# Kernel tuning notes

Hardware: AMD Instinct MI355X
Metric: run time of the kernel (lower is better)

Reference implementation:

```python
import jax, jax.numpy as jnp
import numpy as np

B, S, D, H = 2, 2048, 1024, 16
DH = D // H


def setup_inputs() -> dict:
    key = jax.random.key(0)
    ks = jax.random.split(key, 13)
    s = 1.0 / np.sqrt(D)
    inp = {
        "q": jax.random.normal(ks[0], (B, S, D), jnp.float32),
        "k": jax.random.normal(ks[1], (B, S, D), jnp.float32),
        "v": jax.random.normal(ks[2], (B, S, D), jnp.float32),
        # causal mask [B,1,Q,K]: True = attend
        "attn_mask": jnp.broadcast_to(jnp.tril(jnp.ones((S, S), bool))[None, None], (B, 1, S, S)),
        "rel_bias": 0.1 * jax.random.normal(ks[3], (H, S, S), jnp.float32),
        "Wq": s * jax.random.normal(ks[4], (D, D), jnp.float32),
        "bq": jnp.zeros((D,), jnp.float32),
        "Wk": s * jax.random.normal(ks[5], (D, D), jnp.float32),
        "bk": jnp.zeros((D,), jnp.float32),
        "Wv": s * jax.random.normal(ks[6], (D, D), jnp.float32),
        "bv": jnp.zeros((D,), jnp.float32),
        "Wo": s * jax.random.normal(ks[7], (D, D), jnp.float32),
        "bo": jnp.zeros((D,), jnp.float32),
    }
    return inp


def reference(q, k, v, attn_mask, rel_bias, Wq, bq, Wk, bk, Wv, bv, Wo, bo):
    Bq, Q, Dm = q.shape
    K = k.shape[1]
    # projections -> [B, H, S, DH]
    qh = (q @ Wq + bq).reshape(Bq, Q, H, DH).transpose(0, 2, 1, 3)
    kh = (k @ Wk + bk).reshape(Bq, K, H, DH).transpose(0, 2, 1, 3)
    vh = (v @ Wv + bv).reshape(Bq, K, H, DH).transpose(0, 2, 1, 3)
    scores = jnp.einsum("bhqd,bhkd->bhqk", qh, kh) / np.sqrt(DH).astype(np.float32)
    scores = scores + rel_bias  # [H,Q,K] broadcasts over batch
    scores = jnp.where(attn_mask, scores, -jnp.inf)
    attn = jax.nn.softmax(scores, axis=-1)
    out = jnp.einsum("bhqk,bhkd->bhqd", attn, vh)
    out = out.transpose(0, 2, 1, 3).reshape(Bq, Q, Dm)
    return out @ Wo + bo
```

## Files before the change

### kernel.cpp

```cpp
#include <hip/hip_runtime.h>

typedef unsigned short u16;
typedef __attribute__((ext_vector_type(8))) short bf16x8;
typedef __attribute__((ext_vector_type(4))) float f32x4;
typedef __attribute__((ext_vector_type(4))) unsigned short us4;

#define B_ 2
#define S_ 2048
#define D_ 1024
#define H_ 16
#define DH_ 64
#define M_ 4096

__device__ __forceinline__ u16 f2bf(float f) {
  unsigned int u = __builtin_bit_cast(unsigned int, f);
  u += 0x7FFFu + ((u >> 16) & 1u);
  return (u16)(u >> 16);
}

__device__ __forceinline__ unsigned int cvtpk(float lo, float hi) {
  unsigned int r;
  asm("v_cvt_pk_bf16_f32 %0, %1, %2" : "=v"(r) : "v"(lo), "v"(hi));
  return r;
}

__device__ __forceinline__ float fexp2(float x) {
  float r;
  asm("v_exp_f32 %0, %1" : "=v"(r) : "v"(x));
  return r;
}

__device__ __forceinline__ void gload_lds16(const void* g, void* l) {
  __builtin_amdgcn_global_load_lds(
      (__attribute__((address_space(1))) void*)(g),
      (__attribute__((address_space(3))) void*)(l),
      16, 0, 0);
}

__global__ __launch_bounds__(256) void wprep_kernel(const float* __restrict__ W0,
                                                    const float* __restrict__ W1,
                                                    const float* __restrict__ W2,
                                                    const float* __restrict__ W3,
                                                    u16* __restrict__ Wt,
                                                    const float* __restrict__ qin,
                                                    const float* __restrict__ kin,
                                                    const float* __restrict__ vin,
                                                    u16* __restrict__ Xq,
                                                    u16* __restrict__ Xk,
                                                    u16* __restrict__ Xv) {
  int z = blockIdx.z;
  if (z < 4) {
    __shared__ float tile[32][33];
    const float* W = (z == 0) ? W0 : (z == 1) ? W1 : (z == 2) ? W2 : W3;
    u16* out = Wt + (size_t)z * D_ * D_;
    int tx = threadIdx.x, ty = threadIdx.y;
    int x = blockIdx.x * 32 + tx;
    for (int j = 0; j < 32; j += 8)
      tile[ty + j][tx] = W[(size_t)(blockIdx.y * 32 + ty + j) * D_ + x];
    __syncthreads();
    int x2 = blockIdx.y * 32 + tx;
    for (int j = 0; j < 32; j += 8)
      out[(size_t)(blockIdx.x * 32 + ty + j) * D_ + x2] = f2bf(tile[tx][ty + j]);
  } else {
    int zz = z - 4;
    const float* src = (zz == 0) ? qin : (zz == 1) ? kin : vin;
    u16* dst = (zz == 0) ? Xq : (zz == 1) ? Xk : Xv;
    int bid = blockIdx.y * 32 + blockIdx.x;
    int t = threadIdx.y * 32 + threadIdx.x;
    const float4* s4 = (const float4*)src;
    for (int i = 0; i < 4; ++i) {
      int idx = bid * 1024 + i * 256 + t;
      float4 v4 = s4[idx];
      us4 o;
      o[0] = f2bf(v4.x); o[1] = f2bf(v4.y); o[2] = f2bf(v4.z); o[3] = f2bf(v4.w);
      ((us4*)dst)[idx] = o;
    }
  }
}

__global__ __launch_bounds__(256) void gemm_qkv(const u16* __restrict__ Xq,
                                                const u16* __restrict__ Xk,
                                                const u16* __restrict__ Xv,
                                                const u16* __restrict__ Wt,
                                                const float* __restrict__ bq,
                                                const float* __restrict__ bk,
                                                const float* __restrict__ bv,
                                                u16* __restrict__ Qh,
                                                u16* __restrict__ Kh,
                                                u16* __restrict__ Vt) {
  __shared__ u16 As[128 * 32];
  __shared__ u16 Bs[128 * 32];
  int fid = blockIdx.x;
  int xcd = fid & 7, ii = fid >> 3;
  int grp = ii >> 3, yy = ii & 7;
  int gg = xcd * 12 + grp;
  int z = gg >> 5;
  int xx = gg & 31;
  const u16* A = (z == 0) ? Xq : (z == 1) ? Xk : Xv;
  const u16* Bt = Wt + (size_t)z * D_ * D_;
  const float* bias = (z == 0) ? bq : (z == 1) ? bk : bv;
  u16* O = (z == 0) ? Qh : (z == 1) ? Kh : Vt;

  int tid = threadIdx.x;
  int lane = tid & 63, wave = tid >> 6;
  int m0 = xx * 128, n0 = yy * 128;
  int wr = wave >> 1, wc = wave & 1;
  int fr = lane & 15, fk = (lane >> 4) * 8;

  f32x4 acc[4][4];
  const f32x4 vzero = {0.f, 0.f, 0.f, 0.f};
  for (int i = 0; i < 4; ++i)
    for (int j = 0; j < 4; ++j) acc[i][j] = vzero;

  for (int k0 = 0; k0 < D_; k0 += 32) {
    if (k0) __syncthreads();
    for (int i = 0; i < 2; ++i) {
      int wofs = ((i * 4 + wave) << 10);
      int ofs = wofs + lane * 16;
      int row = ofs >> 6;
      int cole = (ofs & 63) >> 1;
      gload_lds16(A + (size_t)(m0 + row) * D_ + k0 + cole, (char*)As + wofs);
      gload_lds16(Bt + (size_t)(n0 + row) * D_ + k0 + cole, (char*)Bs + wofs);
    }
    __syncthreads();
    bf16x8 af[4], bfr[4];
    for (int mi = 0; mi < 4; ++mi)
      af[mi] = *(const bf16x8*)(As + (wr * 64 + mi * 16 + fr) * 32 + fk);
    for (int ni = 0; ni < 4; ++ni)
      bfr[ni] = *(const bf16x8*)(Bs + (wc * 64 + ni * 16 + fr) * 32 + fk);
    for (int mi = 0; mi < 4; ++mi)
      for (int ni = 0; ni < 4; ++ni)
        acc[mi][ni] =
            __builtin_amdgcn_mfma_f32_16x16x32_bf16(af[mi], bfr[ni], acc[mi][ni], 0, 0, 0);
  }

  if (z == 2) {
    for (int mi = 0; mi < 4; ++mi) {
      int rowb = m0 + wr * 64 + mi * 16 + (lane >> 4) * 4;
      int bb2 = rowb >> 11, s0 = rowb & (S_ - 1);
      for (int ni = 0; ni < 4; ++ni) {
        int col = n0 + wc * 64 + ni * 16 + fr;
        int hh = col >> 6, dh = col & 63;
        float bv = bias[col];
        us4 pk;
        for (int r = 0; r < 4; ++r) pk[r] = f2bf(acc[mi][ni][r] + bv);
        *(us4*)(O + ((size_t)(bb2 * H_ + hh) * DH_ + dh) * S_ + s0) = pk;
      }
    }
  } else {
    float scale = (z == 0) ? 0.125f : 1.0f;
    for (int mi = 0; mi < 4; ++mi) {
      int rowb = m0 + wr * 64 + mi * 16 + (lane >> 4) * 4;
      for (int ni = 0; ni < 4; ++ni) {
        int col = n0 + wc * 64 + ni * 16 + fr;
        int hh = col >> 6, dh = col & 63;
        float bv = bias[col];
        for (int r = 0; r < 4; ++r) {
          int row = rowb + r;
          int bb2 = row >> 11, s = row & (S_ - 1);
          O[((size_t)(bb2 * H_ + hh) * S_ + s) * DH_ + dh] =
              f2bf((acc[mi][ni][r] + bv) * scale);
        }
      }
    }
  }
}

__global__ __launch_bounds__(256) void gemm_out(const u16* __restrict__ A,
                                                const u16* __restrict__ Bt,
                                                const float* __restrict__ bias,
                                                float* __restrict__ O) {
  __shared__ u16 As[64 * 32];
  __shared__ u16 Bs[128 * 32];
  int fid = blockIdx.x;
  int xcd = fid & 7, ii = fid >> 3;
  int grp = ii >> 3, yy = ii & 7;
  int gg = xcd * 8 + grp;
  int tid = threadIdx.x;
  int lane = tid & 63, wave = tid >> 6;
  int m0 = gg * 64, n0 = yy * 128;
  int fr = lane & 15, fk = (lane >> 4) * 8;

  f32x4 acc[4][2];
  const f32x4 vzero = {0.f, 0.f, 0.f, 0.f};
  for (int i = 0; i < 4; ++i)
    for (int j = 0; j < 2; ++j) acc[i][j] = vzero;

  for (int k0 = 0; k0 < D_; k0 += 32) {
    if (k0) __syncthreads();
    {
      int wofs = wave << 10;
      int ofs = wofs + lane * 16;
      int row = ofs >> 6;
      int cole = (ofs & 63) >> 1;
      gload_lds16(A + (size_t)(m0 + row) * D_ + k0 + cole, (char*)As + wofs);
    }
    for (int i = 0; i < 2; ++i) {
      int wofs = ((i * 4 + wave) << 10);
      int ofs = wofs + lane * 16;
      int row = ofs >> 6;
      int cole = (ofs & 63) >> 1;
      gload_lds16(Bt + (size_t)(n0 + row) * D_ + k0 + cole, (char*)Bs + wofs);
    }
    __syncthreads();
    bf16x8 af[4], bfr[2];
    for (int mi = 0; mi < 4; ++mi)
      af[mi] = *(const bf16x8*)(As + (mi * 16 + fr) * 32 + fk);
    for (int ni = 0; ni < 2; ++ni)
      bfr[ni] = *(const bf16x8*)(Bs + (wave * 32 + ni * 16 + fr) * 32 + fk);
    for (int mi = 0; mi < 4; ++mi)
      for (int ni = 0; ni < 2; ++ni)
        acc[mi][ni] =
            __builtin_amdgcn_mfma_f32_16x16x32_bf16(af[mi], bfr[ni], acc[mi][ni], 0, 0, 0);
  }

  for (int mi = 0; mi < 4; ++mi) {
    int rowb = m0 + mi * 16 + (lane >> 4) * 4;
    for (int ni = 0; ni < 2; ++ni) {
      int col = n0 + wave * 32 + ni * 16 + fr;
      float bv = bias[col];
      for (int r = 0; r < 4; ++r)
        O[(size_t)(rowb + r) * D_ + col] = acc[mi][ni][r] + bv;
    }
  }
}

__global__ __launch_bounds__(256, 4) void attn_kernel(const u16* __restrict__ Qh,
                                                      const u16* __restrict__ Kh,
                                                      const u16* __restrict__ Vt,
                                                      const float* __restrict__ relb,
                                                      u16* __restrict__ attnout) {
  __shared__ u16 KVs[2][2][4096];

  int fid = blockIdx.x;
  int rr = fid >> 8, c = fid & 255;
  int j = c >> 3, e = c & 7;
  int s = (rr & 1) ? j : 31 - j;
  int h = (rr & 1) ? e + 8 : e;
  int b = rr >> 1;

  int w = threadIdx.x >> 6, lane = threadIdx.x & 63;
  int fr = lane & 15, g = lane >> 4;
  int q0w = s * 64 + w * 16;
  int qme = q0w + fr;
  int bh = b * H_ + h;
  int sx = (fr & 7) << 4;

  int kind = w >> 1;
  int i0 = (w & 1) * 4;
  int srow_lo = lane >> 3;
  int scb = (lane & 7) * 16;

  const u16* Qb = Qh + ((size_t)bh * S_ + q0w) * DH_;
  bf16x8 qf0 = *(const bf16x8*)(Qb + fr * DH_ + 8 * g);
  bf16x8 qf1 = *(const bf16x8*)(Qb + fr * DH_ + 32 + 8 * g);

  const float* Bq = relb + (size_t)h * S_ * S_ + (size_t)qme * S_ + 4 * g;
  const float LOG2E = 1.44269504f;

  int T = s + 1;

  auto STAGE = [&](int buf, int kb) {
    for (int i = 0; i < 4; ++i) {
      int ii = i0 + i;
      int row = ii * 8 + srow_lo;
      int cbs = scb ^ ((row & 7) << 4);
      const u16* src;
      if (kind == 0)
        src = Kh + ((size_t)bh * S_ + kb + row) * DH_ + (cbs >> 1);
      else
        src = Vt + ((size_t)bh * DH_ + row) * S_ + kb + (cbs >> 1);
      gload_lds16(src, &KVs[kind][buf][ii * 512]);
    }
  };

  f32x4 acc[4];
  const f32x4 vzero = {0.f, 0.f, 0.f, 0.f};
  for (int f4 = 0; f4 < 4; ++f4) acc[f4] = vzero;
  float m = -1.0e4f, l = 0.f;

  STAGE(0, 0);
  f32x4 bi[4], bn[4];
  for (int cc = 0; cc < 4; ++cc) bi[cc] = *(const f32x4*)(Bq + 16 * cc);
  __syncthreads();

  for (int t = 0; t < T; ++t) {
    int kb = t * 64;
    int buf = t & 1;
    bool diag = (t == T - 1);
    if (!diag) {
      STAGE(buf ^ 1, kb + 64);
      for (int cc = 0; cc < 4; ++cc) bn[cc] = *(const f32x4*)(Bq + kb + 64 + 16 * cc);
    }

    const u16* Kt = &KVs[0][buf][0];
    const u16* Vl = &KVs[1][buf][0];

    f32x4 sc[4];
    __builtin_amdgcn_s_setprio(1);
    for (int cc = 0; cc < 4; ++cc) {
      bf16x8 k0 = *(const bf16x8*)(Kt + (16 * cc + fr) * 64 + (((16 * g) ^ sx) >> 1));
      bf16x8 k1 = *(const bf16x8*)(Kt + (16 * cc + fr) * 64 + (((64 + 16 * g) ^ sx) >> 1));
      f32x4 z = __builtin_amdgcn_mfma_f32_16x16x32_bf16(k0, qf0, bi[cc], 0, 0, 0);
      z = __builtin_amdgcn_mfma_f32_16x16x32_bf16(k1, qf1, z, 0, 0, 0);
      sc[cc] = z;
    }
    __builtin_amdgcn_s_setprio(0);
    if (diag) {
      for (int cc = 0; cc < 4; ++cc)
        for (int r = 0; r < 4; ++r) {
          int key = kb + 16 * cc + 4 * g + r;
          sc[cc][r] = (key <= qme) ? sc[cc][r] : -1e30f;
        }
    }
    float pm = sc[0][0];
    for (int cc = 0; cc < 4; ++cc)
      for (int r = 0; r < 4; ++r) pm = fmaxf(pm, sc[cc][r]);
    pm = fmaxf(pm, __shfl_xor(pm, 16));
    pm = fmaxf(pm, __shfl_xor(pm, 32));
    if (!__all(pm - m <= 8.0f)) {
      float mn = fmaxf(m, pm);
      float corr = __expf(m - mn);
      m = mn;
      l *= corr;
      float c0 = __shfl(corr, 4 * g + 0);
      float c1 = __shfl(corr, 4 * g + 1);
      float c2 = __shfl(corr, 4 * g + 2);
      float c3 = __shfl(corr, 4 * g + 3);
      for (int f4 = 0; f4 < 4; ++f4) {
        acc[f4][0] *= c0; acc[f4][1] *= c1; acc[f4][2] *= c2; acc[f4][3] *= c3;
      }
    }
    float nms = m * -LOG2E;
    float rs = 0.f;
    for (int cc = 0; cc < 4; ++cc)
      for (int r = 0; r < 4; ++r) {
        sc[cc][r] = fexp2(fmaf(sc[cc][r], LOG2E, nms));
        rs += sc[cc][r];
      }
    l += rs;
    union { unsigned int w4[4]; bf16x8 v; } pp[2];
    for (int jj = 0; jj < 2; ++jj) {
      pp[jj].w4[0] = cvtpk(sc[2 * jj][0], sc[2 * jj][1]);
      pp[jj].w4[1] = cvtpk(sc[2 * jj][2], sc[2 * jj][3]);
      pp[jj].w4[2] = cvtpk(sc[2 * jj + 1][0], sc[2 * jj + 1][1]);
      pp[jj].w4[3] = cvtpk(sc[2 * jj + 1][2], sc[2 * jj + 1][3]);
    }
    __builtin_amdgcn_s_setprio(1);
    for (int f4 = 0; f4 < 4; ++f4) {
      for (int jj = 0; jj < 2; ++jj) {
        union { us4 hh[2]; bf16x8 v; } vf;
        vf.hh[0] = *(const us4*)(Vl + (f4 * 16 + fr) * 64 + (((jj * 64 + 8 * g) ^ sx) >> 1));
        vf.hh[1] = *(const us4*)(Vl + (f4 * 16 + fr) * 64 + (((jj * 64 + 32 + 8 * g) ^ sx) >> 1));
        acc[f4] = __builtin_amdgcn_mfma_f32_16x16x32_bf16(pp[jj].v, vf.v, acc[f4], 0, 0, 0);
      }
    }
    __builtin_amdgcn_s_setprio(0);
    for (int cc = 0; cc < 4; ++cc) bi[cc] = bn[cc];
    __syncthreads();
  }

  l += __shfl_xor(l, 16);
  l += __shfl_xor(l, 32);
  float il = 1.f / l;
  for (int r = 0; r < 4; ++r) {
    float ilr = __shfl(il, 4 * g + r);
    int qq = q0w + 4 * g + r;
    u16* ob = attnout + ((size_t)b * S_ + qq) * D_ + h * 64;
    for (int f4 = 0; f4 < 4; ++f4) ob[f4 * 16 + fr] = f2bf(acc[f4][r] * ilr);
  }
}

extern "C" void kernel_launch(void* const* d_in, const int* in_sizes, int n_in,
                              void* d_out, int out_size, void* d_ws, size_t ws_size,
                              hipStream_t stream) {
  const float* q = (const float*)d_in[0];
  const float* k = (const float*)d_in[1];
  const float* v = (const float*)d_in[2];
  const float* rb = (const float*)d_in[4];
  const float* Wq = (const float*)d_in[5];
  const float* bq = (const float*)d_in[6];
  const float* Wk = (const float*)d_in[7];
  const float* bk = (const float*)d_in[8];
  const float* Wv = (const float*)d_in[9];
  const float* bv = (const float*)d_in[10];
  const float* Wo = (const float*)d_in[11];
  const float* bo = (const float*)d_in[12];
  float* out = (float*)d_out;

  char* ws = (char*)d_ws;
  const size_t SZ = (size_t)M_ * D_ * 2;
  u16* Xq = (u16*)(ws);
  u16* Xk = (u16*)(ws + SZ);
  u16* Xv = (u16*)(ws + 2 * SZ);
  u16* Qh = (u16*)(ws + 3 * SZ);
  u16* Kh = (u16*)(ws + 4 * SZ);
  u16* Vt = (u16*)(ws + 5 * SZ);
  u16* Wt = (u16*)(ws + 6 * SZ);
  u16* Xb = Xq;

  wprep_kernel<<<dim3(32, 32, 7), dim3(32, 8), 0, stream>>>(Wq, Wk, Wv, Wo, Wt,
                                                            q, k, v, Xq, Xk, Xv);

  gemm_qkv<<<dim3(768), 256, 0, stream>>>(Xq, Xk, Xv, Wt, bq, bk, bv, Qh, Kh, Vt);

  attn_kernel<<<dim3(1024), 256, 0, stream>>>(Qh, Kh, Vt, rb, Xb);

  gemm_out<<<dim3(512), 256, 0, stream>>>(Xb, Wt + 3 * (size_t)D_ * D_, bo, out);
}
```

Baseline: 142.5 us.

## Load K/V fragments directly from global into registers, dropping LDS staging

The attention kernel no longer stages K and V tiles into shared memory with async global-to-LDS copies and block barriers. Each wave now loads its own K and V MFMA fragments straight from global memory into registers, prefetching the next K tile while the current one is used. Launch bounds drop from 4 to 3 blocks per CU to make room for the extra registers. The cost is that all four waves read the same K/V data redundantly from global or L2, with narrower, less coalesced V loads and lower occupancy, in exchange for removing the barriers and LDS traffic.

Measured after the change: 363.9 us. 155% more time.

```diff
diff --git a/kernel.cpp b/kernel.cpp
--- a/kernel.cpp
+++ b/kernel.cpp
@@ -225,13 +225,11 @@
   }
 }
 
-__global__ __launch_bounds__(256, 4) void attn_kernel(const u16* __restrict__ Qh,
+__global__ __launch_bounds__(256, 3) void attn_kernel(const u16* __restrict__ Qh,
                                                       const u16* __restrict__ Kh,
                                                       const u16* __restrict__ Vt,
                                                       const float* __restrict__ relb,
                                                       u16* __restrict__ attnout) {
-  __shared__ u16 KVs[2][2][4096];
-
   int fid = blockIdx.x;
   int rr = fid >> 8, c = fid & 255;
   int j = c >> 3, e = c & 7;
@@ -244,68 +242,62 @@
   int q0w = s * 64 + w * 16;
   int qme = q0w + fr;
   int bh = b * H_ + h;
-  int sx = (fr & 7) << 4;
-
-  int kind = w >> 1;
-  int i0 = (w & 1) * 4;
-  int srow_lo = lane >> 3;
-  int scb = (lane & 7) * 16;
 
   const u16* Qb = Qh + ((size_t)bh * S_ + q0w) * DH_;
   bf16x8 qf0 = *(const bf16x8*)(Qb + fr * DH_ + 8 * g);
   bf16x8 qf1 = *(const bf16x8*)(Qb + fr * DH_ + 32 + 8 * g);
 
+  const u16* Kp = Kh + ((size_t)bh * S_ + fr) * DH_ + 8 * g;
+  const u16* Vp = Vt + ((size_t)bh * DH_ + fr) * S_ + 4 * g;
   const float* Bq = relb + (size_t)h * S_ * S_ + (size_t)qme * S_ + 4 * g;
   const float LOG2E = 1.44269504f;
 
   int T = s + 1;
-
-  auto STAGE = [&](int buf, int kb) {
-    for (int i = 0; i < 4; ++i) {
-      int ii = i0 + i;
-      int row = ii * 8 + srow_lo;
-      int cbs = scb ^ ((row & 7) << 4);
-      const u16* src;
-      if (kind == 0)
-        src = Kh + ((size_t)bh * S_ + kb + row) * DH_ + (cbs >> 1);
-      else
-        src = Vt + ((size_t)bh * DH_ + row) * S_ + kb + (cbs >> 1);
-      gload_lds16(src, &KVs[kind][buf][ii * 512]);
-    }
-  };
 
   f32x4 acc[4];
   const f32x4 vzero = {0.f, 0.f, 0.f, 0.f};
   for (int f4 = 0; f4 < 4; ++f4) acc[f4] = vzero;
   float m = -1.0e4f, l = 0.f;
 
-  STAGE(0, 0);
+  bf16x8 kf0[4], kf1[4];
+  for (int cc = 0; cc < 4; ++cc) {
+    kf0[cc] = *(const bf16x8*)(Kp + (size_t)(16 * cc) * DH_);
+    kf1[cc] = *(const bf16x8*)(Kp + (size_t)(16 * cc) * DH_ + 32);
+  }
   f32x4 bi[4], bn[4];
   for (int cc = 0; cc < 4; ++cc) bi[cc] = *(const f32x4*)(Bq + 16 * cc);
-  __syncthreads();
 
   for (int t = 0; t < T; ++t) {
     int kb = t * 64;
-    int buf = t & 1;
     bool diag = (t == T - 1);
-    if (!diag) {
-      STAGE(buf ^ 1, kb + 64);
-      for (int cc = 0; cc < 4; ++cc) bn[cc] = *(const f32x4*)(Bq + kb + 64 + 16 * cc);
-    }
-
-    const u16* Kt = &KVs[0][buf][0];
-    const u16* Vl = &KVs[1][buf][0];
+
+    us4 vf[4][4];
+    for (int f4 = 0; f4 < 4; ++f4) {
+      const u16* vrow = Vp + (size_t)(f4 * 16) * S_ + kb;
+      vf[f4][0] = *(const us4*)(vrow);
+      vf[f4][1] = *(const us4*)(vrow + 16);
+      vf[f4][2] = *(const us4*)(vrow + 32);
+      vf[f4][3] = *(const us4*)(vrow + 48);
+    }
 
     f32x4 sc[4];
     __builtin_amdgcn_s_setprio(1);
     for (int cc = 0; cc < 4; ++cc) {
-      bf16x8 k0 = *(const bf16x8*)(Kt + (16 * cc + fr) * 64 + (((16 * g) ^ sx) >> 1));
-      bf16x8 k1 = *(const bf16x8*)(Kt + (16 * cc + fr) * 64 + (((64 + 16 * g) ^ sx) >> 1));
-      f32x4 z = __builtin_amdgcn_mfma_f32_16x16x32_bf16(k0, qf0, bi[cc], 0, 0, 0);
-      z = __builtin_amdgcn_mfma_f32_16x16x32_bf16(k1, qf1, z, 0, 0, 0);
+      f32x4 z = __builtin_amdgcn_mfma_f32_16x16x32_bf16(kf0[cc], qf0, bi[cc], 0, 0, 0);
+      z = __builtin_amdgcn_mfma_f32_16x16x32_bf16(kf1[cc], qf1, z, 0, 0, 0);
       sc[cc] = z;
     }
     __builtin_amdgcn_s_setprio(0);
+
+    if (!diag) {
+      const u16* Kn = Kp + (size_t)(kb + 64) * DH_;
+      for (int cc = 0; cc < 4; ++cc) {
+        kf0[cc] = *(const bf16x8*)(Kn + (size_t)(16 * cc) * DH_);
+        kf1[cc] = *(const bf16x8*)(Kn + (size_t)(16 * cc) * DH_ + 32);
+      }
+      for (int cc = 0; cc < 4; ++cc) bn[cc] = *(const f32x4*)(Bq + kb + 64 + 16 * cc);
+    }
+
     if (diag) {
       for (int cc = 0; cc < 4; ++cc)
         for (int r = 0; r < 4; ++r) {
@@ -349,15 +341,14 @@
     __builtin_amdgcn_s_setprio(1);
     for (int f4 = 0; f4 < 4; ++f4) {
       for (int jj = 0; jj < 2; ++jj) {
-        union { us4 hh[2]; bf16x8 v; } vf;
-        vf.hh[0] = *(const us4*)(Vl + (f4 * 16 + fr) * 64 + (((jj * 64 + 8 * g) ^ sx) >> 1));
-        vf.hh[1] = *(const us4*)(Vl + (f4 * 16 + fr) * 64 + (((jj * 64 + 32 + 8 * g) ^ sx) >> 1));
-        acc[f4] = __builtin_amdgcn_mfma_f32_16x16x32_bf16(pp[jj].v, vf.v, acc[f4], 0, 0, 0);
+        union { us4 hh[2]; bf16x8 v; } vv;
+        vv.hh[0] = vf[f4][2 * jj];
+        vv.hh[1] = vf[f4][2 * jj + 1];
+        acc[f4] = __builtin_amdgcn_mfma_f32_16x16x32_bf16(pp[jj].v, vv.v, acc[f4], 0, 0, 0);
       }
     }
     __builtin_amdgcn_s_setprio(0);
     for (int cc = 0; cc < 4; ++cc) bi[cc] = bn[cc];
-    __syncthreads();
   }
 
   l += __shfl_xor(l, 16);
```
